# Kernel optimization log

Hardware: AMD Instinct MI355X
Metric: run time of the kernel (lower is better)

Reference implementation:

```python
import jax, jax.numpy as jnp
import numpy as np

CUBE = (80, 80, 20)
NBINS = CUBE[0] * CUBE[1] * CUBE[2]  # 128000
NVIEW = 5
B = 2
C_IMG, C_FEAT = 3, 32
H_IMG, W_IMG = 512, 512
H_F, W_F = 128, 128
HID = 256
IN_DIM = 3 + 2 * (C_IMG + C_FEAT)  # 73


def setup_inputs() -> dict:
    key = jax.random.key(0)
    ks = jax.random.split(key, 8)
    denorm_imgs = jax.random.uniform(ks[0], (NVIEW, B, C_IMG, H_IMG, W_IMG), jnp.float32)
    feats2d = jax.random.normal(ks[1], (NVIEW, B, C_FEAT, H_F, W_F), jnp.float32)
    # grid_sample coords in [-1, 1], last dim = (x, y)
    sample_grid = jax.random.uniform(ks[2], (NVIEW, NBINS, 2), jnp.float32, -1.0, 1.0)
    points = jax.random.normal(ks[3], (NBINS, 3), jnp.float32)
    W1 = jax.random.normal(ks[4], (IN_DIM, HID), jnp.float32) * (1.0 / np.sqrt(IN_DIM))
    b1 = jnp.zeros((HID,), jnp.float32)
    W2 = jax.random.normal(ks[5], (HID, 1), jnp.float32) * (1.0 / np.sqrt(HID))
    b2 = jnp.zeros((1,), jnp.float32)
    return {"denorm_imgs": denorm_imgs, "feats2d": feats2d, "sample_grid": sample_grid,
            "points": points, "W1": W1, "b1": b1, "W2": W2, "b2": b2}


def _grid_sample(img, grid):
    """Bilinear grid_sample, align_corners=True, padding_mode='zeros'.
    img: [B, C, H, W]; grid: [N, 2] in [-1, 1] (x, y). Returns [B, C, N]."""
    H, W = img.shape[-2], img.shape[-1]
    ix = (grid[:, 0] + 1.0) * 0.5 * (W - 1)
    iy = (grid[:, 1] + 1.0) * 0.5 * (H - 1)
    x0 = jnp.floor(ix)
    y0 = jnp.floor(iy)
    x1 = x0 + 1.0
    y1 = y0 + 1.0
    wx1 = ix - x0
    wx0 = 1.0 - wx1
    wy1 = iy - y0
    wy0 = 1.0 - wy1

    def corner(x, y, w):
        valid = ((x >= 0) & (x <= W - 1) & (y >= 0) & (y <= H - 1)).astype(img.dtype)
        xi = jnp.clip(x, 0, W - 1).astype(jnp.int32)
        yi = jnp.clip(y, 0, H - 1).astype(jnp.int32)
        vals = img[:, :, yi, xi]  # [B, C, N]
        return vals * (w * valid)[None, None, :]

    return (corner(x0, y0, wx0 * wy0) + corner(x1, y0, wx1 * wy0)
            + corner(x0, y1, wx0 * wy1) + corner(x1, y1, wx1 * wy1))


def reference(denorm_imgs, feats2d, sample_grid, points, W1, b1, W2, b2):
    # Batched multi-view grid_sample: [V, B, C, N]
    cubes_img = jax.vmap(_grid_sample)(denorm_imgs, sample_grid)
    cubes_feat = jax.vmap(_grid_sample)(feats2d, sample_grid)
    cubes = jnp.concatenate([cubes_img, cubes_feat], axis=2)  # [V, B, C_tot, N]
    cubes = jnp.transpose(cubes, (1, 2, 3, 0))  # [B, C_tot, N, V]
    nview = cubes.shape[-1]
    mean = jnp.sum(cubes, axis=-1, keepdims=True) / nview          # [B, C, N, 1]
    var = jnp.sum((cubes - mean) ** 2, axis=-1, keepdims=True) / nview
    var = jnp.exp(-var)
    gvol = jnp.concatenate([mean[..., 0], var[..., 0]], axis=1)    # [B, 2C, N]
    feats = jnp.transpose(gvol, (0, 2, 1))                         # [B, N, 2C]
    bsz = feats.shape[0]
    pts = jnp.broadcast_to(points[None], (bsz,) + points.shape)    # [B, N, 3]
    inp = jnp.concatenate([pts, feats], axis=-1)                   # [B, N, 3+2C]
    h = jax.nn.relu(inp @ W1 + b1)
    density = jax.nn.softplus(h @ W2 + b2)                         # [B, N, 1]
    alpha = 1.0 - jnp.exp(-density)
    return alpha.reshape(bsz, 1, CUBE[0], CUBE[1], CUBE[2])
```

## Files before the change

kernel.cpp:

```cpp
#include <hip/hip_runtime.h>

#define NVIEW 5
#define NB    128000
#define CF    32
#define HID   256
#define KA    96
#define IMG_HW 262144
#define FT_HW  16384

typedef __attribute__((ext_vector_type(8))) short short8;
typedef __attribute__((ext_vector_type(4))) float f32x4;

__device__ __forceinline__ unsigned int f2bf(float f) {
    unsigned int u = __float_as_uint(f);
    return (u + 0x7fffu + ((u >> 16) & 1u)) >> 16;
}
__device__ __forceinline__ unsigned int pk(float a, float b) {
    return f2bf(a) | (f2bf(b) << 16);
}
__device__ __forceinline__ float b2f_lo(unsigned int u) { return __uint_as_float(u << 16); }
__device__ __forceinline__ float b2f_hi(unsigned int u) { return __uint_as_float(u & 0xffff0000u); }

__device__ __forceinline__ int mapk(int k) {
    if (k < 22) return k;
    if (k < 25) return k + 16;
    if (k == 25) return -1;
    if (k < 42) return k + 15;
    if (k < 48) return -1;
    if (k < 64) return k - 26;
    if (k < 80) return k - 7;
    return -1;
}

__global__ __launch_bounds__(256) void prep(
    const float* __restrict__ imgs, const float* __restrict__ feats,
    const float* __restrict__ W1, const float* __restrict__ b1,
    const float* __restrict__ W2, const float* __restrict__ b2,
    uint2* __restrict__ imgsP, uint4* __restrict__ featsP,
    unsigned int* __restrict__ Bfrag, float* __restrict__ bw)
{
    const int bidx = blockIdx.x;
    const int t = threadIdx.x;
    if (bidx < 1280) {
        int gid = bidx * 256 + t;
        int v   = gid >> 16;
        int px  = (gid & 65535) * 4;
        const float* base = imgs + (size_t)v * 6 * IMG_HW + px;
        float4 pl[6];
        #pragma unroll
        for (int p = 0; p < 6; p++)
            pl[p] = *(const float4*)(base + (size_t)p * IMG_HW);
        uint2 o[4];
        #pragma unroll
        for (int i = 0; i < 4; i++) {
            unsigned int c[6];
            #pragma unroll
            for (int p = 0; p < 6; p++)
                c[p] = (unsigned int)fminf(((const float*)&pl[p])[i] * 255.f + 0.5f, 255.f);
            o[i].x = c[0] | (c[1] << 8) | (c[2] << 16);
            o[i].y = c[3] | (c[4] << 8) | (c[5] << 16);
        }
        uint4* dst = (uint4*)(imgsP + (size_t)v * IMG_HW + px);
        dst[0] = make_uint4(o[0].x, o[0].y, o[1].x, o[1].y);
        dst[1] = make_uint4(o[2].x, o[2].y, o[3].x, o[3].y);
    } else if (bidx < 2560) {
        __shared__ unsigned short tile[64][65];
        const int pixbase = (bidx - 1280) * 64;
        const int v   = pixbase >> 14;
        const int rem = pixbase & 16383;
        {
            const int p = t & 63;
            const int s = t >> 6;
            #pragma unroll
            for (int it = 0; it < 16; it++) {
                int plane = it * 4 + s;
                tile[plane][p] =
                    (unsigned short)f2bf(feats[((size_t)v * 64 + plane) * FT_HW + rem + p]);
            }
        }
        __syncthreads();
        {
            const int q = t & 7;
            #pragma unroll
            for (int it = 0; it < 2; it++) {
                int p = it * 32 + (t >> 3);
                uint4 o;
                o.x = (unsigned)tile[q * 8 + 0][p] | ((unsigned)tile[q * 8 + 1][p] << 16);
                o.y = (unsigned)tile[q * 8 + 2][p] | ((unsigned)tile[q * 8 + 3][p] << 16);
                o.z = (unsigned)tile[q * 8 + 4][p] | ((unsigned)tile[q * 8 + 5][p] << 16);
                o.w = (unsigned)tile[q * 8 + 6][p] | ((unsigned)tile[q * 8 + 7][p] << 16);
                featsP[(size_t)(pixbase + p) * 8 + q] = o;
            }
        }
    } else {
        int e = (bidx - 2560) * 256 + t;
        int ju = e & 3;
        int nn = (e >> 2) & 255;
        int o  = e >> 10;
        int k0 = o * 8 + ju * 2;
        int i0 = mapk(k0), i1 = mapk(k0 + 1);
        float f0 = (i0 >= 0) ? W1[i0 * 256 + nn] : 0.f;
        float f1 = (i1 >= 0) ? W1[i1 * 256 + nn] : 0.f;
        Bfrag[e] = pk(f0, f1);
        if (e < 256)       bw[e] = b1[e];
        else if (e < 512)  bw[e] = W2[e - 256];
        else if (e == 512) bw[e] = b2[0];
    }
}

#define AROW 13

__global__ __launch_bounds__(256, 2) void fused_gather_mlp(
    const uint2* __restrict__ imgsP,
    const unsigned short* __restrict__ featsP,
    const float* __restrict__ grid,
    const float* __restrict__ points,
    const unsigned int*   __restrict__ Bfrag,
    const float*          __restrict__ bw,
    float* __restrict__ out)
{
    __shared__ unsigned int Bl[12288];
    __shared__ uint4 As4[128 * AROW];
    __shared__ float b1s[HID];
    __shared__ float W2s[HID];

    const int tid = threadIdx.x;

    {
        const uint4* src = (const uint4*)Bfrag;
        uint4* dst = (uint4*)Bl;
        #pragma unroll
        for (int i = 0; i < 12; i++) dst[i * 256 + tid] = src[i * 256 + tid];
        b1s[tid] = bw[tid];
        W2s[tid] = bw[256 + tid];
    }
    const float b2v = bw[512];

    const int n    = blockIdx.x * 64 + (tid >> 2);
    const int b    = (tid >> 1) & 1;
    const int half = tid & 1;

    float sumf[16], ssqf[16];
    #pragma unroll
    for (int c = 0; c < 16; c++) { sumf[c] = 0.f; ssqf[c] = 0.f; }
    float si0 = 0.f, si1 = 0.f, si2 = 0.f;
    float qi0 = 0.f, qi1 = 0.f, qi2 = 0.f;
    float p0 = 0.f, p1 = 0.f, p2 = 0.f;
    if (half == 0) {
        p0 = points[n * 3 + 0];
        p1 = points[n * 3 + 1];
        p2 = points[n * 3 + 2];
    }

    #pragma unroll
    for (int v = 0; v < NVIEW; v++) {
        const float2 g = ((const float2*)grid)[v * NB + n];
        const float gx = g.x, gy = g.y;

        if (half == 0) {
            float ix = (gx + 1.f) * 0.5f * 511.f;
            float iy = (gy + 1.f) * 0.5f * 511.f;
            float x0f = floorf(ix), y0f = floorf(iy);
            float x1f = x0f + 1.f, y1f = y0f + 1.f;
            float wx1 = ix - x0f, wx0 = 1.f - wx1;
            float wy1 = iy - y0f, wy0 = 1.f - wy1;
            float vi0 = 0.f, vi1 = 0.f, vi2 = 0.f;
            const uint2* base = imgsP + (size_t)v * IMG_HW;
            #pragma unroll
            for (int k = 0; k < 4; k++) {
                float xf = (k & 1) ? x1f : x0f;
                float yf = (k >> 1) ? y1f : y0f;
                float w  = ((k & 1) ? wx1 : wx0) * ((k >> 1) ? wy1 : wy0);
                float vd = (xf >= 0.f && xf <= 511.f && yf >= 0.f && yf <= 511.f) ? 1.f : 0.f;
                w *= vd;
                int xi = (int)fminf(fmaxf(xf, 0.f), 511.f);
                int yi = (int)fminf(fmaxf(yf, 0.f), 511.f);
                uint2 iv = base[yi * 512 + xi];
                unsigned int sel = b ? iv.y : iv.x;
                vi0 += w * (float)(sel & 255u);
                vi1 += w * (float)((sel >> 8) & 255u);
                vi2 += w * (float)((sel >> 16) & 255u);
            }
            si0 += vi0; qi0 += vi0 * vi0;
            si1 += vi1; qi1 += vi1 * vi1;
            si2 += vi2; qi2 += vi2 * vi2;
        }

        {
            float ix = (gx + 1.f) * 0.5f * 127.f;
            float iy = (gy + 1.f) * 0.5f * 127.f;
            float x0f = floorf(ix), y0f = floorf(iy);
            float x1f = x0f + 1.f, y1f = y0f + 1.f;
            float wx1 = ix - x0f, wx0 = 1.f - wx1;
            float wy1 = iy - y0f, wy0 = 1.f - wy1;
            const unsigned short* fb =
                featsP + ((size_t)v * FT_HW) * 64 + b * 32 + half * 16;
            float val[16];
            #pragma unroll
            for (int c = 0; c < 16; c++) val[c] = 0.f;
            #pragma unroll
            for (int k = 0; k < 4; k++) {
                float xf = (k & 1) ? x1f : x0f;
                float yf = (k >> 1) ? y1f : y0f;
                float w  = ((k & 1) ? wx1 : wx0) * ((k >> 1) ? wy1 : wy0);
                float vd = (xf >= 0.f && xf <= 127.f && yf >= 0.f && yf <= 127.f) ? 1.f : 0.f;
                w *= vd;
                int xi = (int)fminf(fmaxf(xf, 0.f), 127.f);
                int yi = (int)fminf(fmaxf(yf, 0.f), 127.f);
                const uint4* p = (const uint4*)(fb + (size_t)(yi * 128 + xi) * 64);
                #pragma unroll
                for (int q = 0; q < 2; q++) {
                    uint4 f4 = p[q];
                    val[q * 8 + 0] += w * b2f_lo(f4.x);
                    val[q * 8 + 1] += w * b2f_hi(f4.x);
                    val[q * 8 + 2] += w * b2f_lo(f4.y);
                    val[q * 8 + 3] += w * b2f_hi(f4.y);
                    val[q * 8 + 4] += w * b2f_lo(f4.z);
                    val[q * 8 + 5] += w * b2f_hi(f4.z);
                    val[q * 8 + 6] += w * b2f_lo(f4.w);
                    val[q * 8 + 7] += w * b2f_hi(f4.w);
                }
            }
            #pragma unroll
            for (int c = 0; c < 16; c++) {
                sumf[c] += val[c];
                ssqf[c] += val[c] * val[c];
            }
        }
    }

    #pragma unroll
    for (int c = 0; c < 16; c++) {
        float m = sumf[c] * 0.2f;
        float q = ssqf[c] * 0.2f - m * m;
        sumf[c] = m;
        ssqf[c] = expf(-q);
    }
    const float s1 = 0.2f * (1.f / 255.f);
    const float s2 = 0.2f * (1.f / 65025.f);
    float mi0 = si0 * s1, mi1 = si1 * s1, mi2 = si2 * s1;
    float ei0 = expf(-(qi0 * s2 - mi0 * mi0));
    float ei1 = expf(-(qi1 * s2 - mi1 * mi1));
    float ei2 = expf(-(qi2 * s2 - mi2 * mi2));

    unsigned int u[24];
    if (half == 0) {
        u[0] = pk(p0, p1);
        u[1] = pk(p2, mi0);
        u[2] = pk(mi1, mi2);
        #pragma unroll
        for (int j = 0; j < 8; j++) u[3 + j] = pk(sumf[2 * j], sumf[2 * j + 1]);
        u[11] = pk(ei0, ei1);
        u[12] = pk(ei2, 0.f);
        #pragma unroll
        for (int j = 0; j < 8; j++) u[13 + j] = pk(ssqf[2 * j], ssqf[2 * j + 1]);
        u[21] = 0u; u[22] = 0u; u[23] = 0u;
    } else {
        #pragma unroll
        for (int j = 0; j < 8; j++) u[j]     = pk(sumf[2 * j], sumf[2 * j + 1]);
        #pragma unroll
        for (int j = 0; j < 8; j++) u[8 + j] = pk(ssqf[2 * j], ssqf[2 * j + 1]);
        #pragma unroll
        for (int j = 16; j < 24; j++) u[j] = 0u;
    }

    {
        uint4* arow = &As4[(tid >> 1) * AROW + half * 6];
        #pragma unroll
        for (int i = 0; i < 6; i++)
            arow[i] = make_uint4(u[4 * i], u[4 * i + 1], u[4 * i + 2], u[4 * i + 3]);
    }
    __syncthreads();

    const int w    = tid >> 6;
    const int lane = tid & 63;
    const int col  = lane & 15;
    const int quad = lane >> 4;
    const long rowbase = (long)blockIdx.x * 128 + w * 32;

    f32x4 acc[2][16];
    #pragma unroll
    for (int m = 0; m < 2; m++)
        #pragma unroll
        for (int t = 0; t < 16; t++)
            acc[m][t] = (f32x4){0.f, 0.f, 0.f, 0.f};

    const unsigned int* bp = Bl + (quad * 256 + col) * 4;

    #pragma unroll
    for (int s = 0; s < 3; s++) {
        short8 af0 = *(const short8*)&As4[(w * 32 + col)      * AROW + s * 4 + quad];
        short8 af1 = *(const short8*)&As4[(w * 32 + 16 + col) * AROW + s * 4 + quad];
        #pragma unroll
        for (int t = 0; t < 16; t++) {
            short8 bf = *(const short8*)(bp + s * 4096 + t * 64);
            acc[0][t] = __builtin_amdgcn_mfma_f32_16x16x32_bf16(af0, bf, acc[0][t], 0, 0, 0);
            acc[1][t] = __builtin_amdgcn_mfma_f32_16x16x32_bf16(af1, bf, acc[1][t], 0, 0, 0);
        }
    }

    float pm[2][4] = {{0.f, 0.f, 0.f, 0.f}, {0.f, 0.f, 0.f, 0.f}};
    #pragma unroll
    for (int t = 0; t < 16; t++) {
        float b1v = b1s[t * 16 + col];
        float w2v = W2s[t * 16 + col];
        #pragma unroll
        for (int m = 0; m < 2; m++)
            #pragma unroll
            for (int r = 0; r < 4; r++) {
                float h = fmaxf(acc[m][t][r] + b1v, 0.f);
                pm[m][r] += h * w2v;
            }
    }
    #pragma unroll
    for (int m = 0; m < 2; m++)
        #pragma unroll
        for (int r = 0; r < 4; r++) {
            float p = pm[m][r];
            p += __shfl_xor(p, 1);
            p += __shfl_xor(p, 2);
            p += __shfl_xor(p, 4);
            p += __shfl_xor(p, 8);
            pm[m][r] = p;
        }

    if (col == 0) {
        #pragma unroll
        for (int m = 0; m < 2; m++)
            #pragma unroll
            for (int r = 0; r < 4; r++) {
                float x  = pm[m][r] + b2v;
                float sp = fmaxf(x, 0.f) + log1pf(expf(-fabsf(x)));
                float alpha = -expm1f(-sp);
                long row = rowbase + m * 16 + quad * 4 + r;
                out[(row & 1) * (long)NB + (row >> 1)] = alpha;
            }
    }
}

extern "C" void kernel_launch(void* const* d_in, const int* in_sizes, int n_in,
                              void* d_out, int out_size, void* d_ws, size_t ws_size,
                              hipStream_t stream) {
    const float* imgs   = (const float*)d_in[0];
    const float* feats  = (const float*)d_in[1];
    const float* grid   = (const float*)d_in[2];
    const float* points = (const float*)d_in[3];
    const float* W1     = (const float*)d_in[4];
    const float* b1     = (const float*)d_in[5];
    const float* W2     = (const float*)d_in[6];
    const float* b2     = (const float*)d_in[7];
    float* out = (float*)d_out;

    uint2*          imgsP  = (uint2*)d_ws;
    unsigned short* featsP = (unsigned short*)(imgsP + (size_t)NVIEW * IMG_HW);
    unsigned int*   Bfrag  = (unsigned int*)(featsP + (size_t)NVIEW * FT_HW * 64);
    float*          bwbuf  = (float*)(Bfrag + 12288);

    prep<<<dim3(2608), dim3(256), 0, stream>>>(
        imgs, feats, W1, b1, W2, b2,
        imgsP, (uint4*)featsP, Bfrag, bwbuf);
    fused_gather_mlp<<<dim3(2000), dim3(256), 0, stream>>>(
        imgsP, featsP, grid, points, Bfrag, bwbuf, out);
}
```

Baseline: 190.2 us.

## Alias A-tile and weight LDS buffers and split MLP accumulation into halves

The A-tile staging buffer and the B weight fragments now share one LDS array. A fragments are read into registers before the weights are copied in, with an extra barrier between the two phases. The hidden dimension is processed in two halves of 128, so only 16 accumulator vectors are live instead of 32. Together these cut LDS footprint and register pressure, which could raise occupancy. The cost is an extra __syncthreads, and the weight copy is now serialized after the gather instead of overlapping with it.

```diff
diff --git a/kernel.cpp b/kernel.cpp
--- a/kernel.cpp
+++ b/kernel.cpp
@@ -119,21 +119,13 @@
     const float*          __restrict__ bw,
     float* __restrict__ out)
 {
-    __shared__ unsigned int Bl[12288];
-    __shared__ uint4 As4[128 * AROW];
+    __shared__ unsigned int Lds[12288];
     __shared__ float b1s[HID];
     __shared__ float W2s[HID];
 
     const int tid = threadIdx.x;
-
-    {
-        const uint4* src = (const uint4*)Bfrag;
-        uint4* dst = (uint4*)Bl;
-        #pragma unroll
-        for (int i = 0; i < 12; i++) dst[i * 256 + tid] = src[i * 256 + tid];
-        b1s[tid] = bw[tid];
-        W2s[tid] = bw[256 + tid];
-    }
+    b1s[tid] = bw[tid];
+    W2s[tid] = bw[256 + tid];
     const float b2v = bw[512];
 
     const int n    = blockIdx.x * 64 + (tid >> 2);
@@ -264,13 +256,13 @@
         for (int j = 16; j < 24; j++) u[j] = 0u;
     }
 
+    uint4* As4 = (uint4*)Lds;
     {
         uint4* arow = &As4[(tid >> 1) * AROW + half * 6];
         #pragma unroll
         for (int i = 0; i < 6; i++)
             arow[i] = make_uint4(u[4 * i], u[4 * i + 1], u[4 * i + 2], u[4 * i + 3]);
     }
-    __syncthreads();
 
     const int w    = tid >> 6;
     const int lane = tid & 63;
@@ -278,40 +270,60 @@
     const int quad = lane >> 4;
     const long rowbase = (long)blockIdx.x * 128 + w * 32;
 
-    f32x4 acc[2][16];
-    #pragma unroll
-    for (int m = 0; m < 2; m++)
-        #pragma unroll
-        for (int t = 0; t < 16; t++)
-            acc[m][t] = (f32x4){0.f, 0.f, 0.f, 0.f};
-
-    const unsigned int* bp = Bl + (quad * 256 + col) * 4;
-
+    short8 af[2][3];
     #pragma unroll
     for (int s = 0; s < 3; s++) {
-        short8 af0 = *(const short8*)&As4[(w * 32 + col)      * AROW + s * 4 + quad];
-        short8 af1 = *(const short8*)&As4[(w * 32 + 16 + col) * AROW + s * 4 + quad];
-        #pragma unroll
-        for (int t = 0; t < 16; t++) {
-            short8 bf = *(const short8*)(bp + s * 4096 + t * 64);
-            acc[0][t] = __builtin_amdgcn_mfma_f32_16x16x32_bf16(af0, bf, acc[0][t], 0, 0, 0);
-            acc[1][t] = __builtin_amdgcn_mfma_f32_16x16x32_bf16(af1, bf, acc[1][t], 0, 0, 0);
-        }
-    }
+        af[0][s] = *(const short8*)&As4[(w * 32 + col)      * AROW + s * 4 + quad];
+        af[1][s] = *(const short8*)&As4[(w * 32 + 16 + col) * AROW + s * 4 + quad];
+    }
+
+    __syncthreads();
+
+    {
+        const uint4* src = (const uint4*)Bfrag;
+        uint4* dst = (uint4*)Lds;
+        #pragma unroll
+        for (int i = 0; i < 12; i++) dst[i * 256 + tid] = src[i * 256 + tid];
+    }
+    __syncthreads();
+
+    const unsigned int* bp = Lds + (quad * 256 + col) * 4;
 
     float pm[2][4] = {{0.f, 0.f, 0.f, 0.f}, {0.f, 0.f, 0.f, 0.f}};
     #pragma unroll
-    for (int t = 0; t < 16; t++) {
-        float b1v = b1s[t * 16 + col];
-        float w2v = W2s[t * 16 + col];
+    for (int h = 0; h < 2; h++) {
+        f32x4 acc[2][8];
         #pragma unroll
         for (int m = 0; m < 2; m++)
             #pragma unroll
-            for (int r = 0; r < 4; r++) {
-                float h = fmaxf(acc[m][t][r] + b1v, 0.f);
-                pm[m][r] += h * w2v;
-            }
-    }
+            for (int t = 0; t < 8; t++)
+                acc[m][t] = (f32x4){0.f, 0.f, 0.f, 0.f};
+
+        #pragma unroll
+        for (int s = 0; s < 3; s++) {
+            #pragma unroll
+            for (int t = 0; t < 8; t++) {
+                short8 bf = *(const short8*)(bp + s * 4096 + (h * 8 + t) * 64);
+                acc[0][t] = __builtin_amdgcn_mfma_f32_16x16x32_bf16(af[0][s], bf, acc[0][t], 0, 0, 0);
+                acc[1][t] = __builtin_amdgcn_mfma_f32_16x16x32_bf16(af[1][s], bf, acc[1][t], 0, 0, 0);
+            }
+        }
+
+        #pragma unroll
+        for (int t = 0; t < 8; t++) {
+            int j = h * 128 + t * 16 + col;
+            float b1v = b1s[j];
+            float w2v = W2s[j];
+            #pragma unroll
+            for (int m = 0; m < 2; m++)
+                #pragma unroll
+                for (int r = 0; r < 4; r++) {
+                    float hh = fmaxf(acc[m][t][r] + b1v, 0.f);
+                    pm[m][r] += hh * w2v;
+                }
+        }
+    }
+
     #pragma unroll
     for (int m = 0; m < 2; m++)
         #pragma unroll
```

Result: faster. 186.3 us (-2.1%).
